# Performance work log

Hardware: AMD Instinct MI355X
Metric: run time of the kernel (lower is better)

The kernel has to match this reference:

```python
import jax, jax.numpy as jnp
import numpy as np

E = 800_000      # number of edges
DIN = 128        # in_channels
DMID = 256       # mid_channels
DOUT = 128       # output_channels
V = 50_000       # number of vertices (segments)


def setup_inputs() -> dict:
    key = jax.random.key(0)
    k1, k2, k3, k4, k5 = jax.random.split(key, 5)
    x = jax.random.normal(k1, (E, DIN), dtype=jnp.float32)
    vertex_id = jax.random.randint(k2, (E,), 0, V)
    W1 = jax.random.normal(k3, (DIN, DMID), dtype=jnp.float32) * (1.0 / np.sqrt(DIN))
    b1 = jax.random.normal(k4, (DMID,), dtype=jnp.float32) * 0.01
    W2 = jax.random.normal(k5, (DIN + DMID, DOUT), dtype=jnp.float32) * (1.0 / np.sqrt(DIN + DMID))
    return {"x": x, "vertex_id": vertex_id, "W1": W1, "b1": b1, "W2": W2, "num_vertices": V}


def reference(x, vertex_id, W1, b1, W2, num_vertices):
    # first_process: Linear(DIN -> DMID)                        (E, DMID)
    z = x @ W1 + b1
    # aggregator: scatter_max over vertex segments              (V, DMID)
    z_max = jax.ops.segment_max(z, vertex_id, num_segments=num_vertices)
    # formatter: index_select gather back to edges              (E, DMID)
    z_vertex = jnp.take(z_max, vertex_id, axis=0)
    # merger: concat along feature dim                          (E, DIN+DMID)
    z_merged = jnp.concatenate([x, z_vertex], axis=-1)
    # second_process: Linear(DIN+DMID -> DOUT, bias=False)      (E, DOUT)
    return z_merged @ W2
```

## Files before the change

kernel.cpp:

```cpp
#include <hip/hip_runtime.h>

#define DIN   128
#define DMID  256
#define DOUT  128
#define VNUM  50000

typedef __attribute__((ext_vector_type(8))) __bf16 bf16x8;
typedef __attribute__((ext_vector_type(4))) float  f32x4;

static __device__ __forceinline__ unsigned short b16(float f) {
  union { __bf16 b; unsigned short u; } r; r.b = (__bf16)f; return r.u;
}
static __device__ __forceinline__ unsigned pk2(float lo, float hi) {
  union { __bf16 b[2]; unsigned u; } r;
  r.b[0] = (__bf16)lo; r.b[1] = (__bf16)hi;
  return r.u;
}
static __device__ __forceinline__ unsigned unflip_bits(unsigned m) {
  unsigned mask = ((int)m < 0) ? 0x80000000u : 0xFFFFFFFFu;
  return m ^ mask;
}
static __device__ __forceinline__ unsigned flip32_from16(unsigned m) {
  return (m << 16) | ((m & 0x8000u) ? 0u : 0xFFFFu);
}

#define LBAR() do {                                            \
    __builtin_amdgcn_sched_barrier(0);                         \
    asm volatile("s_waitcnt lgkmcnt(0)" ::: "memory");         \
    __builtin_amdgcn_sched_barrier(0);                         \
    __builtin_amdgcn_s_barrier();                              \
    __builtin_amdgcn_sched_barrier(0);                         \
  } while (0)

__global__ __launch_bounds__(256) void k_zero(uint4* __restrict__ p, int n16) {
  const int stride = gridDim.x * 256;
  const uint4 z = {0u, 0u, 0u, 0u};
  for (int i = blockIdx.x * 256 + threadIdx.x; i < n16; i += stride) p[i] = z;
}

__global__ void k_hist(const int* __restrict__ vid, int* __restrict__ counts, int E) {
  int i = blockIdx.x * blockDim.x + threadIdx.x;
  if (i < E) atomicAdd(counts + vid[i], 1);
}

__global__ __launch_bounds__(256) void k_scan_red(
    const int* __restrict__ cnt, int* __restrict__ bsum, int V) {
  __shared__ int ws[4];
  const int i = blockIdx.x * 256 + threadIdx.x;
  int c = (i < V) ? cnt[i] : 0;
#pragma unroll
  for (int d = 1; d < 64; d <<= 1) c += __shfl_xor(c, d);
  if ((threadIdx.x & 63) == 0) ws[threadIdx.x >> 6] = c;
  __syncthreads();
  if (threadIdx.x == 0) bsum[blockIdx.x] = ws[0] + ws[1] + ws[2] + ws[3];
}

__global__ __launch_bounds__(256) void k_scan_top(int* __restrict__ bsum, int nb) {
  __shared__ int ws[4];
  const int tid = threadIdx.x, lane = tid & 63, wv = tid >> 6;
  int c = (tid < nb) ? bsum[tid] : 0;
  int s = c;
#pragma unroll
  for (int d = 1; d < 64; d <<= 1) {
    int u = __shfl_up(s, d, 64);
    if (lane >= d) s += u;
  }
  if (lane == 63) ws[wv] = s;
  __syncthreads();
  int off = 0;
  for (int k = 0; k < wv; ++k) off += ws[k];
  if (tid < nb) bsum[tid] = off + (s - c);
}

__global__ __launch_bounds__(256) void k_scan_fix(
    int* __restrict__ cursor, const int* __restrict__ bsum, int V) {
  __shared__ int ws[4];
  const int i = blockIdx.x * 256 + threadIdx.x;
  const int lane = threadIdx.x & 63, wv = threadIdx.x >> 6;
  int c = (i < V) ? cursor[i] : 0;
  int s = c;
#pragma unroll
  for (int d = 1; d < 64; d <<= 1) {
    int u = __shfl_up(s, d, 64);
    if (lane >= d) s += u;
  }
  if (lane == 63) ws[wv] = s;
  __syncthreads();
  int off = bsum[blockIdx.x];
  for (int k = 0; k < wv; ++k) off += ws[k];
  if (i < V) cursor[i] = off + (s - c);
}

__global__ void k_scatter(const int* __restrict__ vid, int* __restrict__ cursor,
                          int* __restrict__ sorted, int E) {
  int i = blockIdx.x * blockDim.x + threadIdx.x;
  if (i < E) {
    int v = vid[i];
    int p = atomicAdd(cursor + v, 1);
    sorted[p] = i;
  }
}

__global__ __launch_bounds__(512) void k_gemm1_max(
    const float* __restrict__ x, const int* __restrict__ vid,
    const int* __restrict__ sorted, const float* __restrict__ W1,
    const float* __restrict__ b1, unsigned* __restrict__ zu, int ntiles) {
  __shared__ unsigned short lx[64 * 136];
  __shared__ unsigned short zt[256 * 70];
  __shared__ int lvid[2][64];

  const int tid  = threadIdx.x;
  const int lane = tid & 63;
  const int w    = tid >> 6;
  const int l15  = lane & 15;
  const int l4   = lane >> 4;
  const int row8 = tid >> 3;
  const int s8   = tid & 7;
  const int G    = gridDim.x;

  bf16x8 bfrag[4][2];
  float  bias[2];
#pragma unroll
  for (int ni = 0; ni < 2; ++ni) {
    const int col = w * 32 + ni * 16 + l15;
    bias[ni] = b1[col];
#pragma unroll
    for (int kk = 0; kk < 4; ++kk) {
      union { bf16x8 v; unsigned short u[8]; } tmp;
#pragma unroll
      for (int j = 0; j < 8; ++j)
        tmp.u[j] = b16(W1[(kk * 32 + l4 * 8 + j) * DMID + col]);
      bfrag[kk][ni] = tmp.v;
    }
  }

  const int t0 = blockIdx.x;
  if (t0 >= ntiles) return;

  {
    if (tid < 64) lvid[0][tid] = vid[sorted[t0 * 64 + tid]];
    const int eid = sorted[t0 * 64 + row8];
    const float4* src =
        reinterpret_cast<const float4*>(x + (size_t)eid * DIN + s8 * 16);
#pragma unroll
    for (int i = 0; i < 4; ++i) {
      float4 v = src[i];
      uint2 o = { pk2(v.x, v.y), pk2(v.z, v.w) };
      *reinterpret_cast<uint2*>(&lx[row8 * 136 + s8 * 16 + i * 4]) = o;
    }
  }
  int eidN = 0, sidN = 0;
  bool moreP = (t0 + G) < ntiles;
  if (moreP) {
    eidN = sorted[(t0 + G) * 64 + row8];
    if (tid < 64) sidN = sorted[(t0 + G) * 64 + tid];
  }
  __syncthreads();

  int cur = 0;
  for (int t = t0; t < ntiles; t += G, cur ^= 1) {
    const bool more1 = (t + G) < ntiles;
    float4 x0, x1, x2, x3;
    int vN = 0;
    if (more1) {
      const float4* src =
          reinterpret_cast<const float4*>(x + (size_t)eidN * DIN + s8 * 16);
      x0 = src[0]; x1 = src[1]; x2 = src[2]; x3 = src[3];
      if (tid < 64) vN = vid[sidN];
    }
    const bool more2 = (t + 2 * G) < ntiles;
    int eidN2 = 0, sidN2 = 0;
    if (more2) {
      eidN2 = sorted[(t + 2 * G) * 64 + row8];
      if (tid < 64) sidN2 = sorted[(t + 2 * G) * 64 + tid];
    }

    const int myv = lvid[cur][lane];
    const int nv  = (lane == 63) ? (myv ^ 1) : lvid[cur][lane + 1];
    const unsigned long long emask = __ballot(myv != nv);
    const bool contOpen = (lvid[cur][31] == lvid[cur][32]);

    f32x4 acc[4][2];
#pragma unroll
    for (int mi = 0; mi < 4; ++mi)
#pragma unroll
      for (int ni = 0; ni < 2; ++ni)
        acc[mi][ni] = (f32x4){bias[ni], bias[ni], bias[ni], bias[ni]};
#pragma unroll
    for (int kk = 0; kk < 4; ++kk) {
      bf16x8 a[4];
#pragma unroll
      for (int mi = 0; mi < 4; ++mi)
        a[mi] = *reinterpret_cast<const bf16x8*>(
            &lx[(mi * 16 + l15) * 136 + kk * 32 + l4 * 8]);
#pragma unroll
      for (int mi = 0; mi < 4; ++mi)
#pragma unroll
        for (int ni = 0; ni < 2; ++ni)
          acc[mi][ni] = __builtin_amdgcn_mfma_f32_16x16x32_bf16(
              a[mi], bfrag[kk][ni], acc[mi][ni], 0, 0, 0);
    }

    {
      unsigned* ztw = reinterpret_cast<unsigned*>(zt);
#pragma unroll
      for (int ni = 0; ni < 2; ++ni) {
        const int col = w * 32 + ni * 16 + l15;
        const int cb  = col * 35 + l4 * 2;
#pragma unroll
        for (int mi = 0; mi < 4; ++mi)
#pragma unroll
          for (int p = 0; p < 2; ++p) {
            unsigned tpk = pk2(acc[mi][ni][2 * p], acc[mi][ni][2 * p + 1]);
            unsigned mflip = 0x80008000u + ((tpk >> 15) & 0x00010001u) * 0x7FFFu;
            ztw[cb + mi * 8 + p] = tpk ^ mflip;
          }
      }
    }
    LBAR();

    if (more1) {
      uint2 o0 = { pk2(x0.x, x0.y), pk2(x0.z, x0.w) };
      uint2 o1 = { pk2(x1.x, x1.y), pk2(x1.z, x1.w) };
      uint2 o2 = { pk2(x2.x, x2.y), pk2(x2.z, x2.w) };
      uint2 o3 = { pk2(x3.x, x3.y), pk2(x3.z, x3.w) };
      unsigned short* dst = &lx[row8 * 136 + s8 * 16];
      *reinterpret_cast<uint2*>(dst + 0)  = o0;
      *reinterpret_cast<uint2*>(dst + 4)  = o1;
      *reinterpret_cast<uint2*>(dst + 8)  = o2;
      *reinterpret_cast<uint2*>(dst + 12) = o3;
      if (tid < 64) lvid[cur ^ 1][tid] = vN;
    }
    __builtin_amdgcn_sched_barrier(0);

    {
      const int col = tid & 255;
      const int h   = tid >> 8;
      const unsigned* zc = reinterpret_cast<const unsigned*>(&zt[col * 70 + h * 32]);
      unsigned curm = 0;
      bool first = true;
#pragma unroll
      for (int p = 0; p < 16; ++p) {
        const unsigned pr = zc[p];
#pragma unroll
        for (int j = 0; j < 2; ++j) {
          const unsigned val = j ? (pr >> 16) : (pr & 0xFFFFu);
          curm = val > curm ? val : curm;
          const int row = h * 32 + p * 2 + j;
          if ((emask >> row) & 1) {
            const int v = lvid[cur][row];
            const unsigned enc = flip32_from16(curm);
            unsigned* ad = zu + (size_t)v * DMID + col;
            if (row == 63 || (first && (h == 0 || contOpen))) atomicMax(ad, enc);
            else *ad = enc;
            curm = 0; first = false;
          }
        }
      }
      if (h == 0 && !((emask >> 31) & 1)) {
        const int v = lvid[cur][31];
        atomicMax(zu + (size_t)v * DMID + col, flip32_from16(curm));
      }
    }
    eidN = eidN2; sidN = sidN2;
    LBAR();
  }
}

__global__ __launch_bounds__(256) void k_ymm(
    const unsigned* __restrict__ zu, const float* __restrict__ W2,
    float* __restrict__ Y, int ntiles) {
  extern __shared__ unsigned short sm[];
  unsigned short* w2bt = sm;
  unsigned short* za   = sm + 128 * 264;

  const int tid  = threadIdx.x;
  const int lane = tid & 63;
  const int w    = tid >> 6;
  const int wr   = w >> 1, wc = w & 1;
  const int l15  = lane & 15, l4 = lane >> 4;

  {
    const int n = tid & 127, kh = tid >> 7;
    for (int k = kh * 128; k < kh * 128 + 128; ++k)
      w2bt[n * 264 + k] = b16(W2[(size_t)(DIN + k) * DOUT + n]);
  }
  __syncthreads();

  for (int t = blockIdx.x; t < ntiles; t += gridDim.x) {
    {
      const int row = tid >> 2, q = tid & 3;
      const int v = t * 64 + row;
      unsigned short* dz = &za[row * 264 + q * 64];
      if (v < VNUM) {
        const uint4* sz = reinterpret_cast<const uint4*>(zu + (size_t)v * DMID + q * 64);
#pragma unroll
        for (int i = 0; i < 16; ++i) {
          uint4 m = sz[i];
          ushort4 o = { (unsigned short)(unflip_bits(m.x) >> 16),
                        (unsigned short)(unflip_bits(m.y) >> 16),
                        (unsigned short)(unflip_bits(m.z) >> 16),
                        (unsigned short)(unflip_bits(m.w) >> 16) };
          *reinterpret_cast<ushort4*>(dz + i * 4) = o;
        }
      } else {
        ushort4 zo = {0, 0, 0, 0};
#pragma unroll
        for (int i = 0; i < 16; ++i) *reinterpret_cast<ushort4*>(dz + i * 4) = zo;
      }
    }
    __syncthreads();

    f32x4 acc[2][4];
#pragma unroll
    for (int mi = 0; mi < 2; ++mi)
#pragma unroll
      for (int ni = 0; ni < 4; ++ni) acc[mi][ni] = (f32x4){0.f, 0.f, 0.f, 0.f};

#pragma unroll
    for (int kk = 0; kk < 8; ++kk) {
      bf16x8 a[2], b[4];
#pragma unroll
      for (int mi = 0; mi < 2; ++mi)
        a[mi] = *reinterpret_cast<const bf16x8*>(
            &za[(wr * 32 + mi * 16 + l15) * 264 + kk * 32 + l4 * 8]);
#pragma unroll
      for (int ni = 0; ni < 4; ++ni)
        b[ni] = *reinterpret_cast<const bf16x8*>(
            &w2bt[(wc * 64 + ni * 16 + l15) * 264 + kk * 32 + l4 * 8]);
#pragma unroll
      for (int mi = 0; mi < 2; ++mi)
#pragma unroll
        for (int ni = 0; ni < 4; ++ni)
          acc[mi][ni] = __builtin_amdgcn_mfma_f32_16x16x32_bf16(
              a[mi], b[ni], acc[mi][ni], 0, 0, 0);
    }

#pragma unroll
    for (int mi = 0; mi < 2; ++mi)
#pragma unroll
      for (int r = 0; r < 4; ++r) {
        const int v = t * 64 + wr * 32 + mi * 16 + l4 * 4 + r;
        if (v < VNUM) {
          float* o = Y + (size_t)v * DOUT + wc * 64 + l15;
#pragma unroll
          for (int ni = 0; ni < 4; ++ni) o[ni * 16] = acc[mi][ni][r];
        }
      }
    __syncthreads();
  }
}

__global__ __launch_bounds__(256, 3) void k_gemm2(
    const float* __restrict__ x, const int* __restrict__ vid,
    const float* __restrict__ W2, const float* __restrict__ Y,
    float* __restrict__ out, int ntiles) {
  __shared__ unsigned short w2at[128 * 136];
  __shared__ unsigned short lx[64 * 136];
  __shared__ int lvid[64];

  const int tid  = threadIdx.x;
  const int lane = tid & 63;
  const int w    = tid >> 6;
  const int wr   = w >> 1, wc = w & 1;
  const int l15  = lane & 15, l4 = lane >> 4;

  {
    const int n = tid & 127, kh = tid >> 7;
    for (int k = kh * 64; k < kh * 64 + 64; ++k)
      w2at[n * 136 + k] = b16(W2[(size_t)k * DOUT + n]);
  }
  __syncthreads();

  for (int t = blockIdx.x; t < ntiles; t += gridDim.x) {
    {
      const int row = tid >> 2, q = tid & 3;
      const float4* sx =
          reinterpret_cast<const float4*>(x + (size_t)(t * 64 + row) * DIN + q * 32);
#pragma unroll
      for (int i = 0; i < 8; ++i) {
        float4 v = sx[i];
        uint2 o = { pk2(v.x, v.y), pk2(v.z, v.w) };
        *reinterpret_cast<uint2*>(&lx[row * 136 + q * 32 + i * 4]) = o;
      }
      if (tid < 64) lvid[tid] = vid[t * 64 + tid];
    }
    __syncthreads();

    float yv[2][4][4];
#pragma unroll
    for (int mi = 0; mi < 2; ++mi)
#pragma unroll
      for (int r = 0; r < 4; ++r) {
        const int row = wr * 32 + mi * 16 + l4 * 4 + r;
        const float* Yr = Y + (size_t)lvid[row] * DOUT + wc * 64 + l15;
#pragma unroll
        for (int ni = 0; ni < 4; ++ni) yv[mi][r][ni] = Yr[ni * 16];
      }

    f32x4 acc[2][4];
#pragma unroll
    for (int mi = 0; mi < 2; ++mi)
#pragma unroll
      for (int ni = 0; ni < 4; ++ni) acc[mi][ni] = (f32x4){0.f, 0.f, 0.f, 0.f};

#pragma unroll
    for (int kk = 0; kk < 4; ++kk) {
      bf16x8 a[2], b[4];
#pragma unroll
      for (int mi = 0; mi < 2; ++mi)
        a[mi] = *reinterpret_cast<const bf16x8*>(
            &lx[(wr * 32 + mi * 16 + l15) * 136 + kk * 32 + l4 * 8]);
#pragma unroll
      for (int ni = 0; ni < 4; ++ni)
        b[ni] = *reinterpret_cast<const bf16x8*>(
            &w2at[(wc * 64 + ni * 16 + l15) * 136 + kk * 32 + l4 * 8]);
#pragma unroll
      for (int mi = 0; mi < 2; ++mi)
#pragma unroll
        for (int ni = 0; ni < 4; ++ni)
          acc[mi][ni] = __builtin_amdgcn_mfma_f32_16x16x32_bf16(
              a[mi], b[ni], acc[mi][ni], 0, 0, 0);
    }

#pragma unroll
    for (int mi = 0; mi < 2; ++mi)
#pragma unroll
      for (int r = 0; r < 4; ++r) {
        const int row = wr * 32 + mi * 16 + l4 * 4 + r;
        float* o = out + (size_t)(t * 64 + row) * DOUT + wc * 64 + l15;
#pragma unroll
        for (int ni = 0; ni < 4; ++ni) o[ni * 16] = acc[mi][ni][r] + yv[mi][r][ni];
      }
    __syncthreads();
  }
}

extern "C" void kernel_launch(void* const* d_in, const int* in_sizes, int n_in,
                              void* d_out, int out_size, void* d_ws, size_t ws_size,
                              hipStream_t stream) {
  const float* x   = (const float*)d_in[0];
  const int*   vid = (const int*)d_in[1];
  const float* W1  = (const float*)d_in[2];
  const float* b1  = (const float*)d_in[3];
  const float* W2  = (const float*)d_in[4];
  float* out = (float*)d_out;

  const int E = in_sizes[1];
  const int ntiles = E / 64;
  const int ntY = (VNUM + 63) / 64;
  const int nb = (VNUM + 255) / 256;

  char* ws = (char*)d_ws;
  size_t off = 0;
  unsigned* zu = (unsigned*)(ws + off); off += (size_t)VNUM * DMID * 4;
  int* cnt     = (int*)(ws + off);      off += (size_t)VNUM * 4;
  int* sorted  = (int*)(ws + off);      off += (size_t)E * 4;
  float* Y     = (float*)(ws + off);    off += (size_t)VNUM * DOUT * 4;
  int* bsum    = (int*)(ws + off);      off += 4096;

  const int n16 = (int)(((size_t)VNUM * DMID * 4 + VNUM * 4) / 16);
  k_zero<<<2048, 256, 0, stream>>>((uint4*)zu, n16);

  k_hist<<<(E + 255) / 256, 256, 0, stream>>>(vid, cnt, E);
  k_scan_red<<<nb, 256, 0, stream>>>(cnt, bsum, VNUM);
  k_scan_top<<<1, 256, 0, stream>>>(bsum, nb);
  k_scan_fix<<<nb, 256, 0, stream>>>(cnt, bsum, VNUM);
  k_scatter<<<(E + 255) / 256, 256, 0, stream>>>(vid, cnt, sorted, E);

  k_gemm1_max<<<512, 512, 0, stream>>>(x, vid, sorted, W1, b1, zu, ntiles);

  const int smY = (128 * 264 + 64 * 264) * sizeof(unsigned short);
  hipFuncSetAttribute((const void*)k_ymm,
                      hipFuncAttributeMaxDynamicSharedMemorySize, smY);
  k_ymm<<<782, 256, smY, stream>>>(zu, W2, Y, ntY);

  k_gemm2<<<768, 256, 0, stream>>>(x, vid, W2, Y, out, ntiles);
}
```

Measured before the change: 586.8 us.

## Shrink gemm1_max edge tile to 32 rows with 256-thread blocks

Restructures the fused first GEMM plus segment-max kernel to process 32-edge tiles with 256 threads, where each wave covers 64 output columns and each thread scans one full column of the tile. The transposed staging buffer becomes a 32-bit padded layout, and the cross-half continuation logic and its extra atomic are removed. Twice as many blocks are launched, so less LDS is used per block and occupancy may rise. In exchange there are more tile boundaries and so more atomicMax traffic. The gemm2 loop's block barriers are also swapped for the LBAR macro.

```diff
diff --git a/kernel.cpp b/kernel.cpp
--- a/kernel.cpp
+++ b/kernel.cpp
@@ -101,13 +101,13 @@
   }
 }
 
-__global__ __launch_bounds__(512) void k_gemm1_max(
+__global__ __launch_bounds__(256) void k_gemm1_max(
     const float* __restrict__ x, const int* __restrict__ vid,
     const int* __restrict__ sorted, const float* __restrict__ W1,
     const float* __restrict__ b1, unsigned* __restrict__ zu, int ntiles) {
-  __shared__ unsigned short lx[64 * 136];
-  __shared__ unsigned short zt[256 * 70];
-  __shared__ int lvid[2][64];
+  __shared__ unsigned short lx[32 * 136];
+  __shared__ unsigned zt[256 * 17];
+  __shared__ int lvid[2][32];
 
   const int tid  = threadIdx.x;
   const int lane = tid & 63;
@@ -118,11 +118,11 @@
   const int s8   = tid & 7;
   const int G    = gridDim.x;
 
-  bf16x8 bfrag[4][2];
-  float  bias[2];
-#pragma unroll
-  for (int ni = 0; ni < 2; ++ni) {
-    const int col = w * 32 + ni * 16 + l15;
+  bf16x8 bfrag[4][4];
+  float  bias[4];
+#pragma unroll
+  for (int ni = 0; ni < 4; ++ni) {
+    const int col = w * 64 + ni * 16 + l15;
     bias[ni] = b1[col];
 #pragma unroll
     for (int kk = 0; kk < 4; ++kk) {
@@ -138,8 +138,8 @@
   if (t0 >= ntiles) return;
 
   {
-    if (tid < 64) lvid[0][tid] = vid[sorted[t0 * 64 + tid]];
-    const int eid = sorted[t0 * 64 + row8];
+    if (tid < 32) lvid[0][tid] = vid[sorted[t0 * 32 + tid]];
+    const int eid = sorted[t0 * 32 + row8];
     const float4* src =
         reinterpret_cast<const float4*>(x + (size_t)eid * DIN + s8 * 16);
 #pragma unroll
@@ -150,10 +150,9 @@
     }
   }
   int eidN = 0, sidN = 0;
-  bool moreP = (t0 + G) < ntiles;
-  if (moreP) {
-    eidN = sorted[(t0 + G) * 64 + row8];
-    if (tid < 64) sidN = sorted[(t0 + G) * 64 + tid];
+  if ((t0 + G) < ntiles) {
+    eidN = sorted[(t0 + G) * 32 + row8];
+    if (tid < 32) sidN = sorted[(t0 + G) * 32 + tid];
   }
   __syncthreads();
 
@@ -166,56 +165,53 @@
       const float4* src =
           reinterpret_cast<const float4*>(x + (size_t)eidN * DIN + s8 * 16);
       x0 = src[0]; x1 = src[1]; x2 = src[2]; x3 = src[3];
-      if (tid < 64) vN = vid[sidN];
+      if (tid < 32) vN = vid[sidN];
     }
     const bool more2 = (t + 2 * G) < ntiles;
     int eidN2 = 0, sidN2 = 0;
     if (more2) {
-      eidN2 = sorted[(t + 2 * G) * 64 + row8];
-      if (tid < 64) sidN2 = sorted[(t + 2 * G) * 64 + tid];
-    }
-
-    const int myv = lvid[cur][lane];
-    const int nv  = (lane == 63) ? (myv ^ 1) : lvid[cur][lane + 1];
-    const unsigned long long emask = __ballot(myv != nv);
-    const bool contOpen = (lvid[cur][31] == lvid[cur][32]);
-
-    f32x4 acc[4][2];
-#pragma unroll
-    for (int mi = 0; mi < 4; ++mi)
-#pragma unroll
-      for (int ni = 0; ni < 2; ++ni)
+      eidN2 = sorted[(t + 2 * G) * 32 + row8];
+      if (tid < 32) sidN2 = sorted[(t + 2 * G) * 32 + tid];
+    }
+
+    const int r32  = lane & 31;
+    const int myv  = lvid[cur][r32];
+    const int nv   = (r32 == 31) ? (myv ^ 1) : lvid[cur][r32 + 1];
+    const unsigned emask = (unsigned)(__ballot(myv != nv) & 0xFFFFFFFFull);
+
+    f32x4 acc[2][4];
+#pragma unroll
+    for (int mi = 0; mi < 2; ++mi)
+#pragma unroll
+      for (int ni = 0; ni < 4; ++ni)
         acc[mi][ni] = (f32x4){bias[ni], bias[ni], bias[ni], bias[ni]};
 #pragma unroll
     for (int kk = 0; kk < 4; ++kk) {
-      bf16x8 a[4];
-#pragma unroll
-      for (int mi = 0; mi < 4; ++mi)
+      bf16x8 a[2];
+#pragma unroll
+      for (int mi = 0; mi < 2; ++mi)
         a[mi] = *reinterpret_cast<const bf16x8*>(
             &lx[(mi * 16 + l15) * 136 + kk * 32 + l4 * 8]);
 #pragma unroll
-      for (int mi = 0; mi < 4; ++mi)
-#pragma unroll
-        for (int ni = 0; ni < 2; ++ni)
+      for (int mi = 0; mi < 2; ++mi)
+#pragma unroll
+        for (int ni = 0; ni < 4; ++ni)
           acc[mi][ni] = __builtin_amdgcn_mfma_f32_16x16x32_bf16(
               a[mi], bfrag[kk][ni], acc[mi][ni], 0, 0, 0);
     }
 
-    {
-      unsigned* ztw = reinterpret_cast<unsigned*>(zt);
-#pragma unroll
-      for (int ni = 0; ni < 2; ++ni) {
-        const int col = w * 32 + ni * 16 + l15;
-        const int cb  = col * 35 + l4 * 2;
-#pragma unroll
-        for (int mi = 0; mi < 4; ++mi)
-#pragma unroll
-          for (int p = 0; p < 2; ++p) {
-            unsigned tpk = pk2(acc[mi][ni][2 * p], acc[mi][ni][2 * p + 1]);
-            unsigned mflip = 0x80008000u + ((tpk >> 15) & 0x00010001u) * 0x7FFFu;
-            ztw[cb + mi * 8 + p] = tpk ^ mflip;
-          }
-      }
+#pragma unroll
+    for (int ni = 0; ni < 4; ++ni) {
+      const int col = w * 64 + ni * 16 + l15;
+      const int cb  = col * 17 + l4 * 2;
+#pragma unroll
+      for (int mi = 0; mi < 2; ++mi)
+#pragma unroll
+        for (int p = 0; p < 2; ++p) {
+          unsigned tpk = pk2(acc[mi][ni][2 * p], acc[mi][ni][2 * p + 1]);
+          unsigned mflip = 0x80008000u + ((tpk >> 15) & 0x00010001u) * 0x7FFFu;
+          zt[cb + mi * 8 + p] = tpk ^ mflip;
+        }
     }
     LBAR();
 
@@ -229,14 +225,13 @@
       *reinterpret_cast<uint2*>(dst + 4)  = o1;
       *reinterpret_cast<uint2*>(dst + 8)  = o2;
       *reinterpret_cast<uint2*>(dst + 12) = o3;
-      if (tid < 64) lvid[cur ^ 1][tid] = vN;
+      if (tid < 32) lvid[cur ^ 1][tid] = vN;
     }
     __builtin_amdgcn_sched_barrier(0);
 
     {
-      const int col = tid & 255;
-      const int h   = tid >> 8;
-      const unsigned* zc = reinterpret_cast<const unsigned*>(&zt[col * 70 + h * 32]);
+      const int col = tid;
+      const unsigned* zc = &zt[col * 17];
       unsigned curm = 0;
       bool first = true;
 #pragma unroll
@@ -246,20 +241,16 @@
         for (int j = 0; j < 2; ++j) {
           const unsigned val = j ? (pr >> 16) : (pr & 0xFFFFu);
           curm = val > curm ? val : curm;
-          const int row = h * 32 + p * 2 + j;
+          const int row = p * 2 + j;
           if ((emask >> row) & 1) {
             const int v = lvid[cur][row];
             const unsigned enc = flip32_from16(curm);
             unsigned* ad = zu + (size_t)v * DMID + col;
-            if (row == 63 || (first && (h == 0 || contOpen))) atomicMax(ad, enc);
+            if (first || row == 31) atomicMax(ad, enc);
             else *ad = enc;
             curm = 0; first = false;
           }
         }
-      }
-      if (h == 0 && !((emask >> 31) & 1)) {
-        const int v = lvid[cur][31];
-        atomicMax(zu + (size_t)v * DMID + col, flip32_from16(curm));
       }
     }
     eidN = eidN2; sidN = sidN2;
@@ -385,7 +376,7 @@
       }
       if (tid < 64) lvid[tid] = vid[t * 64 + tid];
     }
-    __syncthreads();
+    LBAR();
 
     float yv[2][4][4];
 #pragma unroll
@@ -432,7 +423,7 @@
 #pragma unroll
         for (int ni = 0; ni < 4; ++ni) o[ni * 16] = acc[mi][ni][r] + yv[mi][r][ni];
       }
-    __syncthreads();
+    LBAR();
   }
 }
 
@@ -447,7 +438,8 @@
   float* out = (float*)d_out;
 
   const int E = in_sizes[1];
-  const int ntiles = E / 64;
+  const int ntiles32 = E / 32;
+  const int ntiles64 = E / 64;
   const int ntY = (VNUM + 63) / 64;
   const int nb = (VNUM + 255) / 256;
 
@@ -468,12 +460,12 @@
   k_scan_fix<<<nb, 256, 0, stream>>>(cnt, bsum, VNUM);
   k_scatter<<<(E + 255) / 256, 256, 0, stream>>>(vid, cnt, sorted, E);
 
-  k_gemm1_max<<<512, 512, 0, stream>>>(x, vid, sorted, W1, b1, zu, ntiles);
+  k_gemm1_max<<<1024, 256, 0, stream>>>(x, vid, sorted, W1, b1, zu, ntiles32);
 
   const int smY = (128 * 264 + 64 * 264) * sizeof(unsigned short);
   hipFuncSetAttribute((const void*)k_ymm,
                       hipFuncAttributeMaxDynamicSharedMemorySize, smY);
   k_ymm<<<782, 256, smY, stream>>>(zu, W2, Y, ntY);
 
-  k_gemm2<<<768, 256, 0, stream>>>(x, vid, W2, Y, out, ntiles);
-}
+  k_gemm2<<<768, 256, 0, stream>>>(x, vid, W2, Y, out, ntiles64);
+}
```

After: 566.6 us. -3.5%, faster.
